# Optimization experiments

Measured on AMD Instinct MI355X. Metric: run time of the kernel, lower is better.

## Reference

```python
import jax, jax.numpy as jnp
import numpy as np

DIM = 1024
EMSIZE = 64  # per-head dim (cfg.emsize = split_size)
N_HEADS = DIM // EMSIZE


def setup_inputs() -> dict:
    key = jax.random.key(0)
    k1, k2, k3 = jax.random.split(key, 3)
    x = jax.random.normal(k1, (4, 2048, DIM), dtype=jnp.float32)
    w_qkv = jax.random.normal(k2, (DIM, 3 * DIM), dtype=jnp.float32) * 0.02
    b_qkv = jnp.zeros((3 * DIM,), dtype=jnp.float32)
    w_proj = jax.random.normal(k3, (DIM, DIM), dtype=jnp.float32) * 0.02
    b_proj = jnp.zeros((DIM,), dtype=jnp.float32)
    return {"x": x, "w_qkv": w_qkv, "b_qkv": b_qkv, "w_proj": w_proj, "b_proj": b_proj}


def reference(x, w_qkv, b_qkv, w_proj, b_proj):
    B, S, D = x.shape
    H, Dh = N_HEADS, EMSIZE
    # QKV projection (Conv1D = affine on last dim)
    qkv = x @ w_qkv + b_qkv                      # [B, S, 3D]
    q, k, v = jnp.split(qkv, 3, axis=-1)
    # split heads: [B, S, H, Dh] -> [B, H, S, Dh]
    q = q.reshape(B, S, H, Dh).transpose(0, 2, 1, 3)
    k = k.reshape(B, S, H, Dh).transpose(0, 2, 1, 3)
    v = v.reshape(B, S, H, Dh).transpose(0, 2, 1, 3)
    # scaled dot-product attention with causal mask (diag included)
    w = jnp.einsum('bhqd,bhkd->bhqk', q, k) / jnp.sqrt(jnp.float32(Dh))
    causal = jnp.arange(S)[None, :] <= jnp.arange(S)[:, None]  # [S, S]
    w = jnp.where(causal[None, None, :, :], w, jnp.float32(-1e9))
    w = jax.nn.softmax(w, axis=-1)
    # dropout is identity at inference
    a = jnp.einsum('bhqk,bhkd->bhqd', w, v)      # [B, H, S, Dh]
    # merge heads
    a = a.transpose(0, 2, 1, 3).reshape(B, S, D)
    # output projection
    return a @ w_proj + b_proj
```

## Files before the change

### kernel.cpp

```cpp
#include <hip/hip_runtime.h>


typedef __bf16 bf16x8 __attribute__((ext_vector_type(8)));
typedef float f32x4 __attribute__((ext_vector_type(4)));
typedef float f32x8 __attribute__((ext_vector_type(8)));
typedef float f32x16 __attribute__((ext_vector_type(16)));
typedef unsigned int u32;
typedef u32 u32x4 __attribute__((ext_vector_type(4)));
typedef unsigned short u16;

#define QSCALE 0.18033688011112042f

__device__ __forceinline__ u16 f2bf(float f) {
  unsigned u = __builtin_bit_cast(unsigned, f);
  return (u16)((u + 0x7FFFu + ((u >> 16) & 1u)) >> 16);
}

__device__ __forceinline__ u32 cvt_pk_bf16(float lo, float hi) {
  u32 r;
  asm("v_cvt_pk_bf16_f32 %0, %1, %2" : "=v"(r) : "v"(lo), "v"(hi));
  return r;
}

__device__ __forceinline__ void gload16(const void* g, void* l) {
  __builtin_amdgcn_global_load_lds(
      (const __attribute__((address_space(1))) unsigned*)g,
      (__attribute__((address_space(3))) unsigned*)l, 16, 0, 0);
}

__global__ __launch_bounds__(256) void k_cvt(const float4* __restrict__ in,
                                             ushort4* __restrict__ out, int n4) {
  int i = blockIdx.x * 256 + threadIdx.x;
  if (i < n4) {
    float4 v = in[i];
    out[i] = make_ushort4(f2bf(v.x), f2bf(v.y), f2bf(v.z), f2bf(v.w));
  }
}

__global__ __launch_bounds__(256) void k_transpose(const float* __restrict__ in,
                                                   u16* __restrict__ out, int R, int C) {
  __shared__ u16 tile[32][33];
  int c0 = blockIdx.x * 32, r0 = blockIdx.y * 32;
  int tx = threadIdx.x & 31, ty = threadIdx.x >> 5;
  for (int i = 0; i < 32; i += 8)
    tile[ty + i][tx] = f2bf(in[(size_t)(r0 + ty + i) * C + c0 + tx]);
  __syncthreads();
  for (int i = 0; i < 32; i += 8)
    out[(size_t)(c0 + ty + i) * R + r0 + tx] = tile[tx][ty + i];
}

template <int MODE>
__global__ __launch_bounds__(256, 2) void k_gemm(
    const u16* __restrict__ A, const u16* __restrict__ Bt,
    const float* __restrict__ bias, float* __restrict__ outF,
    u16* __restrict__ qb, u16* __restrict__ kb, u16* __restrict__ vb,
    int M, int N, int K) {
  __shared__ u16 sA[128 * 32];
  __shared__ u16 sB[128 * 32];
  const int nTn = N >> 7;
  const int tm = blockIdx.x / nTn, tn = blockIdx.x % nTn;
  const int t = threadIdx.x, w = t >> 6, lane = t & 63, g = lane >> 4, c = lane & 15;
  const int wr = w >> 1, wc = w & 1;
  const int rowA0 = tm << 7, colB0 = tn << 7;
  f32x4 acc[4][4] = {};
  const int r = t >> 2, c8 = (t & 3) << 3;
  const u16* gA = A + (size_t)(rowA0 + r) * K + c8;
  const u16* gB = Bt + (size_t)(colB0 + r) * K + c8;
  char* lA = (char*)sA + w * 1024;
  char* lB = (char*)sB + w * 1024;
  for (int k0 = 0; k0 < K; k0 += 32) {
    __syncthreads();
    gload16(gA + k0, lA);
    gload16(gA + k0 + (size_t)64 * K, lA + 4096);
    gload16(gB + k0, lB);
    gload16(gB + k0 + (size_t)64 * K, lB + 4096);
    __syncthreads();
    bf16x8 af[4], bfr[4];
#pragma unroll
    for (int mi = 0; mi < 4; mi++)
      af[mi] = *(const bf16x8*)&sA[(wr * 64 + mi * 16 + c) * 32 + g * 8];
#pragma unroll
    for (int ni = 0; ni < 4; ni++)
      bfr[ni] = *(const bf16x8*)&sB[(wc * 64 + ni * 16 + c) * 32 + g * 8];
#pragma unroll
    for (int mi = 0; mi < 4; mi++)
#pragma unroll
      for (int ni = 0; ni < 4; ni++)
        acc[mi][ni] = __builtin_amdgcn_mfma_f32_16x16x32_bf16(af[mi], bfr[ni], acc[mi][ni], 0, 0, 0);
  }
#pragma unroll
  for (int mi = 0; mi < 4; mi++) {
    int row0 = rowA0 + wr * 64 + mi * 16 + g * 4;
#pragma unroll
    for (int ni = 0; ni < 4; ni++) {
      int col = colB0 + wc * 64 + ni * 16 + c;
      float bv = bias[col];
      if (MODE == 1) {
#pragma unroll
        for (int i = 0; i < 4; i++)
          outF[(size_t)(row0 + i) * N + col] = acc[mi][ni][i] + bv;
      } else {
        int which = col >> 10, cc = col & 1023, h = cc >> 6, d = cc & 63;
        int b_ = row0 >> 11, s = row0 & 2047;
        size_t bh = (size_t)(b_ * 16 + h);
        if (which == 0) {
          u16* dst = qb + (bh * 2048 + s) * 64 + d;
#pragma unroll
          for (int i = 0; i < 4; i++) dst[(size_t)i * 64] = f2bf((acc[mi][ni][i] + bv) * QSCALE);
        } else if (which == 1) {
          u16* dst = kb + (bh * 2048 + s) * 64 + d;
#pragma unroll
          for (int i = 0; i < 4; i++) dst[(size_t)i * 64] = f2bf(acc[mi][ni][i] + bv);
        } else {
          ushort4 pk = make_ushort4(f2bf(acc[mi][ni][0] + bv), f2bf(acc[mi][ni][1] + bv),
                                    f2bf(acc[mi][ni][2] + bv), f2bf(acc[mi][ni][3] + bv));
          *(ushort4*)&vb[(bh * 64 + d) * 2048 + s] = pk;
        }
      }
    }
  }
}

__global__ __launch_bounds__(256, 4) void k_attn(const u16* __restrict__ qb,
                                                 const u16* __restrict__ kb,
                                                 const u16* __restrict__ vb,
                                                 u16* __restrict__ ab) {
  __shared__ u16 sK[2][64 * 64];
  __shared__ u16 sV[2][64 * 64];
  const int bid = blockIdx.x;
  const int qt = 15 - (bid >> 6), bh = bid & 63;
  const int b_ = bh >> 4, hh = bh & 15;
  const int t = threadIdx.x, w = t >> 6, lane = t & 63;
  const int l31 = lane & 31, h = lane >> 5;
  const int q0 = qt << 7, myq = q0 + w * 32;
  const u16* Kg = kb + (size_t)bh * 2048 * 64;
  const u16* Vg = vb + (size_t)bh * 64 * 2048;
  const int rr = t >> 3, p = t & 7;

  const u16* Qrow = qb + ((size_t)bh * 2048 + myq + l31) * 64;
  bf16x8 qf[4];
#pragma unroll
  for (int ks = 0; ks < 4; ks++) qf[ks] = *(const bf16x8*)&Qrow[ks * 16 + h * 8];

#define STAGE(buf, kv0_)                                                      \
  {                                                                           \
    _Pragma("unroll") for (int i = 0; i < 2; i++) {                           \
      int row = i * 32 + rr;                                                  \
      gload16(Kg + ((size_t)(kv0_) + row) * 64 + ((p ^ (row & 7)) << 3),      \
              (char*)sK[buf] + i * 4096 + w * 1024);                          \
      gload16(Vg + (size_t)row * 2048 + (kv0_) + ((p ^ (row & 7)) << 3),      \
              (char*)sV[buf] + i * 4096 + w * 1024);                          \
    }                                                                         \
  }

  f32x16 ot[2] = {};
  float mrun = -__builtin_inff(), lrun = 0.f;
  const int nt = qt * 2 + 2;

  STAGE(0, 0);
  for (int tt = 0; tt < nt; ++tt) {
    const int kv0 = tt << 6;
    __syncthreads();
    if (tt + 1 < nt) STAGE((tt + 1) & 1, kv0 + 64);
    if (kv0 > myq + 31) continue;
    const char* bK = (const char*)sK[tt & 1];
    const char* bV = (const char*)sV[tt & 1];

    f32x16 st[2] = {};
    __builtin_amdgcn_s_setprio(1);
#pragma unroll
    for (int ks = 0; ks < 4; ks++)
#pragma unroll
      for (int kvt = 0; kvt < 2; kvt++) {
        int row = kvt * 32 + l31;
        bf16x8 kf = *(const bf16x8*)(bK + row * 128 + ((ks * 32 + h * 16) ^ ((row & 7) << 4)));
        st[kvt] = __builtin_amdgcn_mfma_f32_32x32x16_bf16(kf, qf[ks], st[kvt], 0, 0, 0);
      }
    __builtin_amdgcn_s_setprio(0);

    if (kv0 + 63 > myq) {
      const int qm = myq + l31 - kv0 - 4 * h;
#pragma unroll
      for (int kvt = 0; kvt < 2; kvt++)
#pragma unroll
        for (int r = 0; r < 16; r++) {
          const int kvo = kvt * 32 + (r & 3) + 8 * (r >> 2);
          st[kvt][r] = (kvo <= qm) ? st[kvt][r] : -__builtin_inff();
        }
    }

    float mt = -__builtin_inff();
#pragma unroll
    for (int r = 0; r < 16; r++) mt = fmaxf(mt, fmaxf(st[0][r], st[1][r]));
    mt = fmaxf(mt, __shfl_xor(mt, 32, 64));
    float mnew = mrun;
    if (!__all(mt <= mrun + 8.f)) {
      mnew = fmaxf(mrun, mt);
      const float corr = __builtin_amdgcn_exp2f(mrun - mnew);
      lrun *= corr;
#pragma unroll
      for (int df = 0; df < 2; df++) ot[df] *= corr;
      mrun = mnew;
    }
#pragma unroll
    for (int kvt = 0; kvt < 2; kvt++)
#pragma unroll
      for (int r = 0; r < 16; r++) st[kvt][r] = __builtin_amdgcn_exp2f(st[kvt][r] - mnew);
    f32x16 ssum = st[0] + st[1];
    f32x8 t8 = __builtin_shufflevector(ssum, ssum, 0, 1, 2, 3, 4, 5, 6, 7) +
               __builtin_shufflevector(ssum, ssum, 8, 9, 10, 11, 12, 13, 14, 15);
    f32x4 t4 = __builtin_shufflevector(t8, t8, 0, 1, 2, 3) +
               __builtin_shufflevector(t8, t8, 4, 5, 6, 7);
    float lt = (t4[0] + t4[1]) + (t4[2] + t4[3]);
    lt += __shfl_xor(lt, 32, 64);
    lrun += lt;

    u32 pk[2][8];
#pragma unroll
    for (int kvt = 0; kvt < 2; kvt++)
#pragma unroll
      for (int j = 0; j < 8; j++)
        pk[kvt][j] = cvt_pk_bf16(st[kvt][2 * j], st[kvt][2 * j + 1]);
    __builtin_amdgcn_s_setprio(1);
#pragma unroll
    for (int s = 0; s < 4; s++) {
      const int kvf = s >> 1, jb = (s & 1) * 4;
      const u32 XloW0 = pk[kvf][jb + 0], XloW1 = pk[kvf][jb + 1];
      const u32 XhiW0 = pk[kvf][jb + 2], XhiW1 = pk[kvf][jb + 3];
      const u32 cHi0 = (u32)__shfl_xor((int)XhiW0, 32, 64);
      const u32 cHi1 = (u32)__shfl_xor((int)XhiW1, 32, 64);
      const u32 cLo0 = (u32)__shfl_xor((int)XloW0, 32, 64);
      const u32 cLo1 = (u32)__shfl_xor((int)XloW1, 32, 64);
      u32x4 pw;
      pw[0] = h ? cHi0 : XloW0;
      pw[1] = h ? cHi1 : XloW1;
      pw[2] = h ? XhiW0 : cLo0;
      pw[3] = h ? XhiW1 : cLo1;
      const bf16x8 pf = __builtin_bit_cast(bf16x8, pw);
#pragma unroll
      for (int df = 0; df < 2; df++) {
        const int row = df * 32 + l31;
        bf16x8 vf = *(const bf16x8*)(bV + row * 128 + ((s * 32 + h * 16) ^ ((row & 7) << 4)));
        ot[df] = __builtin_amdgcn_mfma_f32_32x32x16_bf16(vf, pf, ot[df], 0, 0, 0);
      }
    }
    __builtin_amdgcn_s_setprio(0);
  }

  const float inv = 1.f / lrun;
  u16* Arow = ab + ((size_t)b_ * 2048 + myq + l31) * 1024 + hh * 64;
#pragma unroll
  for (int df = 0; df < 2; df++)
#pragma unroll
    for (int qd = 0; qd < 4; qd++) {
      const int d0 = df * 32 + qd * 8 + h * 4;
      ushort4 pkv = make_ushort4(f2bf(ot[df][qd * 4 + 0] * inv), f2bf(ot[df][qd * 4 + 1] * inv),
                                 f2bf(ot[df][qd * 4 + 2] * inv), f2bf(ot[df][qd * 4 + 3] * inv));
      *(ushort4*)&Arow[d0] = pkv;
    }
#undef STAGE
}

extern "C" void kernel_launch(void* const* d_in, const int* in_sizes, int n_in,
                              void* d_out, int out_size, void* d_ws, size_t ws_size,
                              hipStream_t stream) {
  const float* x = (const float*)d_in[0];
  const float* w_qkv = (const float*)d_in[1];
  const float* b_qkv = (const float*)d_in[2];
  const float* w_proj = (const float*)d_in[3];
  const float* b_proj = (const float*)d_in[4];

  u16* xb = (u16*)d_ws;
  u16* wqkvT = xb + (size_t)8192 * 1024;
  u16* wprojT = wqkvT + (size_t)3072 * 1024;
  u16* qb = wprojT + (size_t)1024 * 1024;
  u16* kb = qb + (size_t)8192 * 1024;
  u16* vb = kb + (size_t)8192 * 1024;
  u16* ab = xb;

  k_cvt<<<8192, 256, 0, stream>>>((const float4*)x, (ushort4*)xb, 8192 * 1024 / 4);
  k_transpose<<<dim3(3072 / 32, 1024 / 32), 256, 0, stream>>>(w_qkv, wqkvT, 1024, 3072);
  k_transpose<<<dim3(1024 / 32, 1024 / 32), 256, 0, stream>>>(w_proj, wprojT, 1024, 1024);
  k_gemm<0><<<(8192 / 128) * (3072 / 128), 256, 0, stream>>>(
      xb, wqkvT, b_qkv, nullptr, qb, kb, vb, 8192, 3072, 1024);
  k_attn<<<1024, 256, 0, stream>>>(qb, kb, vb, ab);
  k_gemm<1><<<(8192 / 128) * (1024 / 128), 256, 0, stream>>>(
      ab, wprojT, b_proj, (float*)d_out, nullptr, nullptr, nullptr, 8192, 1024, 1024);
}
```

Baseline: 260.8 us.

## Replace QKV GEMM with 256x256-tile double-buffered ping-pong MFMA kernel

```diff
diff --git a/kernel.cpp b/kernel.cpp
--- a/kernel.cpp
+++ b/kernel.cpp
@@ -49,11 +49,150 @@
     out[(size_t)(c0 + ty + i) * R + r0 + tx] = tile[tx][ty + i];
 }
 
+__global__ __launch_bounds__(512, 2) void k_gemm256(
+    const u16* __restrict__ A, const u16* __restrict__ Bt,
+    const float* __restrict__ bias,
+    u16* __restrict__ qb, u16* __restrict__ kb, u16* __restrict__ vb, int K) {
+  __shared__ u16 lds[2][2][2][8192];
+  const int b0 = blockIdx.x;
+  const int bsw = (b0 & 7) * 48 + (b0 >> 3);
+  const int tm = bsw / 12, tn = bsw % 12;
+  const int t = threadIdx.x, w = t >> 6, lane = t & 63;
+  const int wm = w >> 2, wn = w & 3, hb = wn >> 1;
+  const int cls = wm * 2 + hb;
+  const int l31 = lane & 31, h8 = lane >> 5;
+  const int sg8 = ((lane & 7) ^ (lane >> 3)) << 3;
+  const int NT = K >> 6;
+  const u16* Ag = A + (size_t)tm * 256 * K;
+  const u16* Bg = Bt + (size_t)tn * 256 * K;
+
+  f32x16 acc[4][2] = {};
+  bf16x8 aR[4][4], bR[2][4];
+
+#define STAGE_HALF(P, Tn)                                                     \
+  {                                                                           \
+    const u16* gb = ((P)&1) ? Bg : Ag;                                        \
+    _Pragma("unroll") for (int r = 0; r < 2; r++) {                           \
+      int row = r * 64 + w * 8 + (lane >> 3);                                 \
+      gload16(gb + (size_t)(((P) >> 1) * 128 + row) * K + (Tn)*64 + sg8,      \
+              (char*)&lds[(Tn)&1][(P)&1][(P) >> 1][0] + r * 8192 + w * 1024); \
+    }                                                                         \
+  }
+#define LDA(mg)                                                                \
+  _Pragma("unroll") for (int mf = (mg)*2; mf < (mg)*2 + 2; mf++)               \
+  _Pragma("unroll") for (int ks = 0; ks < 4; ks++)                             \
+    aR[mf][ks] = *(const bf16x8*)(Abase + (mf * 32 + l31) * 128 +              \
+                                  (((ks * 2 + h8) ^ (l31 & 7)) << 4));
+#define LDB(nf)                                                                \
+  _Pragma("unroll") for (int ks = 0; ks < 4; ks++)                             \
+    bR[nf][ks] = *(const bf16x8*)(Bbase + ((wn & 1) * 64 + (nf)*32 + l31) * 128 + \
+                                  (((ks * 2 + h8) ^ (l31 & 7)) << 4));
+#define MQ(mg, nf)                                                             \
+  {                                                                            \
+    __builtin_amdgcn_s_setprio(1);                                             \
+    _Pragma("unroll") for (int mf = (mg)*2; mf < (mg)*2 + 2; mf++)             \
+    _Pragma("unroll") for (int ks = 0; ks < 4; ks++)                           \
+      acc[mf][nf] = __builtin_amdgcn_mfma_f32_32x32x16_bf16(                   \
+          aR[mf][ks], bR[nf][ks], acc[mf][nf], 0, 0, 0);                       \
+    __builtin_amdgcn_s_setprio(0);                                             \
+  }
+#define PH(P, QBODY)                                                           \
+  {                                                                            \
+    if (T + 1 < NT) {                                                          \
+      STAGE_HALF(P, T + 1);                                                    \
+      asm volatile("s_waitcnt vmcnt(6)" ::: "memory");                         \
+    } else {                                                                   \
+      if ((P) == 0) asm volatile("s_waitcnt vmcnt(4)" ::: "memory");           \
+      else if ((P) == 1) asm volatile("s_waitcnt vmcnt(2)" ::: "memory");      \
+      else if ((P) == 2) asm volatile("s_waitcnt vmcnt(0)" ::: "memory");      \
+    }                                                                          \
+    __builtin_amdgcn_sched_barrier(0);                                         \
+    __builtin_amdgcn_s_barrier();                                              \
+    __builtin_amdgcn_sched_barrier(0);                                         \
+    const char* Abase = (const char*)&lds[T & 1][0][wm][0];                    \
+    const char* Bbase = (const char*)&lds[T & 1][1][hb][0];                    \
+    (void)Abase; (void)Bbase;                                                  \
+    QBODY                                                                      \
+    asm volatile("s_waitcnt lgkmcnt(0)" ::: "memory");                         \
+    __builtin_amdgcn_sched_barrier(0);                                         \
+    __builtin_amdgcn_s_barrier();                                              \
+    __builtin_amdgcn_sched_barrier(0);                                         \
+  }
+
+  STAGE_HALF(0, 0);
+  STAGE_HALF(1, 0);
+  STAGE_HALF(2, 0);
+  STAGE_HALF(3, 0);
+
+  for (int T = 0; T < NT; ++T) {
+    PH(0, {
+      if (cls == 0)      { LDA(0); LDB(0); MQ(0, 0); }
+      else if (cls == 2) { if (T) MQ(1, 0); }
+      else               { if (T) MQ(1, 1); }
+    })
+    PH(1, {
+      if (cls == 0)      { LDB(1); MQ(0, 1); }
+      else if (cls == 2) { LDA(0); LDB(0); MQ(0, 0); }
+      else               { if (T) MQ(1, 0); }
+    })
+    PH(2, {
+      if (cls == 0)      { LDA(1); MQ(1, 1); }
+      else if (cls == 2) { LDB(1); MQ(0, 1); }
+      else               { LDA(0); LDB(0); MQ(0, 0); }
+    })
+    PH(3, {
+      if (cls == 0)      { MQ(1, 0); }
+      else if (cls == 2) { LDA(1); MQ(1, 1); }
+      else               { LDA(1); LDB(1); MQ(0, 1); }
+    })
+  }
+  if (cls == 2) { MQ(1, 0); }
+  else if (cls == 1 || cls == 3) { MQ(1, 1); MQ(1, 0); }
+
+  const int which = tn >> 2;
+#pragma unroll
+  for (int mf = 0; mf < 4; mf++) {
+    const int rb = tm * 256 + wm * 128 + mf * 32 + 4 * h8;
+    const int b_ = rb >> 11, sB = rb & 2047;
+#pragma unroll
+    for (int nf = 0; nf < 2; nf++) {
+      const int cl = tn * 256 + wn * 64 + nf * 32 + l31;
+      const float bv = bias[cl];
+      const int hd = (cl >> 6) & 15, d = cl & 63;
+      const size_t bh = (size_t)(b_ * 16 + hd);
+      if (which == 0) {
+        u16* dst = qb + (bh * 2048 + sB) * 64 + d;
+#pragma unroll
+        for (int r = 0; r < 16; r++)
+          dst[(size_t)((r & 3) + 8 * (r >> 2)) * 64] = f2bf((acc[mf][nf][r] + bv) * QSCALE);
+      } else if (which == 1) {
+        u16* dst = kb + (bh * 2048 + sB) * 64 + d;
+#pragma unroll
+        for (int r = 0; r < 16; r++)
+          dst[(size_t)((r & 3) + 8 * (r >> 2)) * 64] = f2bf(acc[mf][nf][r] + bv);
+      } else {
+        u16* dst = vb + (bh * 64 + d) * 2048 + sB;
+#pragma unroll
+        for (int rq = 0; rq < 4; rq++) {
+          ushort4 pk = make_ushort4(
+              f2bf(acc[mf][nf][rq * 4 + 0] + bv), f2bf(acc[mf][nf][rq * 4 + 1] + bv),
+              f2bf(acc[mf][nf][rq * 4 + 2] + bv), f2bf(acc[mf][nf][rq * 4 + 3] + bv));
+          *(ushort4*)&dst[rq * 8] = pk;
+        }
+      }
+    }
+  }
+#undef STAGE_HALF
+#undef LDA
+#undef LDB
+#undef MQ
+#undef PH
+}
+
 template <int MODE>
 __global__ __launch_bounds__(256, 2) void k_gemm(
     const u16* __restrict__ A, const u16* __restrict__ Bt,
     const float* __restrict__ bias, float* __restrict__ outF,
-    u16* __restrict__ qb, u16* __restrict__ kb, u16* __restrict__ vb,
     int M, int N, int K) {
   __shared__ u16 sA[128 * 32];
   __shared__ u16 sB[128 * 32];
@@ -95,28 +234,9 @@
     for (int ni = 0; ni < 4; ni++) {
       int col = colB0 + wc * 64 + ni * 16 + c;
       float bv = bias[col];
-      if (MODE == 1) {
-#pragma unroll
-        for (int i = 0; i < 4; i++)
-          outF[(size_t)(row0 + i) * N + col] = acc[mi][ni][i] + bv;
-      } else {
-        int which = col >> 10, cc = col & 1023, h = cc >> 6, d = cc & 63;
-        int b_ = row0 >> 11, s = row0 & 2047;
-        size_t bh = (size_t)(b_ * 16 + h);
-        if (which == 0) {
-          u16* dst = qb + (bh * 2048 + s) * 64 + d;
-#pragma unroll
-          for (int i = 0; i < 4; i++) dst[(size_t)i * 64] = f2bf((acc[mi][ni][i] + bv) * QSCALE);
-        } else if (which == 1) {
-          u16* dst = kb + (bh * 2048 + s) * 64 + d;
-#pragma unroll
-          for (int i = 0; i < 4; i++) dst[(size_t)i * 64] = f2bf(acc[mi][ni][i] + bv);
-        } else {
-          ushort4 pk = make_ushort4(f2bf(acc[mi][ni][0] + bv), f2bf(acc[mi][ni][1] + bv),
-                                    f2bf(acc[mi][ni][2] + bv), f2bf(acc[mi][ni][3] + bv));
-          *(ushort4*)&vb[(bh * 64 + d) * 2048 + s] = pk;
-        }
-      }
+#pragma unroll
+      for (int i = 0; i < 4; i++)
+        outF[(size_t)(row0 + i) * N + col] = acc[mi][ni][i] + bv;
     }
   }
 }
@@ -281,9 +401,8 @@
   k_cvt<<<8192, 256, 0, stream>>>((const float4*)x, (ushort4*)xb, 8192 * 1024 / 4);
   k_transpose<<<dim3(3072 / 32, 1024 / 32), 256, 0, stream>>>(w_qkv, wqkvT, 1024, 3072);
   k_transpose<<<dim3(1024 / 32, 1024 / 32), 256, 0, stream>>>(w_proj, wprojT, 1024, 1024);
-  k_gemm<0><<<(8192 / 128) * (3072 / 128), 256, 0, stream>>>(
-      xb, wqkvT, b_qkv, nullptr, qb, kb, vb, 8192, 3072, 1024);
+  k_gemm256<<<384, 512, 0, stream>>>(xb, wqkvT, b_qkv, qb, kb, vb, 1024);
   k_attn<<<1024, 256, 0, stream>>>(qb, kb, vb, ab);
   k_gemm<1><<<(8192 / 128) * (1024 / 128), 256, 0, stream>>>(
-      ab, wprojT, b_proj, (float*)d_out, nullptr, nullptr, nullptr, 8192, 1024, 1024);
-}
+      ab, wprojT, b_proj, (float*)d_out, 8192, 1024, 1024);
+}
```

Measured after the change: 267.2 us. 1.02x slower.

## Replace QKV GEMM with 256x256-tile double-buffered 32x32 MFMA kernel

Applied to the files above, without the earlier changes.

```diff
diff --git a/kernel.cpp b/kernel.cpp
--- a/kernel.cpp
+++ b/kernel.cpp
@@ -49,11 +49,130 @@
     out[(size_t)(c0 + ty + i) * R + r0 + tx] = tile[tx][ty + i];
 }
 
+__global__ __launch_bounds__(512, 2) void k_gemm256(
+    const u16* __restrict__ A, const u16* __restrict__ Bt,
+    const float* __restrict__ bias,
+    u16* __restrict__ qb, u16* __restrict__ kb, u16* __restrict__ vb) {
+  const int K = 1024, NT = 16;
+  __shared__ u16 lds[2][2][2][8192];
+  const int b0 = blockIdx.x;
+  const int bsw = (b0 & 7) * 48 + (b0 >> 3);
+  const int tm = bsw / 12, tn = bsw % 12;
+  const int t = threadIdx.x, w = t >> 6, lane = t & 63;
+  const int wm = w >> 2, wn = w & 3, hb = wn >> 1;
+  const int l31 = lane & 31, h8 = lane >> 5;
+  const int sg8 = ((lane & 7) ^ ((lane >> 3) & 7)) << 3;
+  const u16* Ag = A + (size_t)tm * 256 * K;
+  const u16* Bg = Bt + (size_t)tn * 256 * K;
+
+  f32x16 acc[4][2] = {};
+  bf16x8 aR[4][4], bR[2][4];
+
+#define STG(ab, hf, Tn, BUF)                                                \
+  { const u16* gb = (ab) ? Bg : Ag;                                         \
+    _Pragma("unroll") for (int r = 0; r < 2; r++) {                         \
+      int row = r * 64 + w * 8 + ((lane >> 3) & 7);                         \
+      gload16(gb + (size_t)((hf)*128 + row) * K + (size_t)(Tn)*64 + sg8,    \
+              (char*)&lds[BUF][ab][hf][0] + r * 8192 + w * 1024);           \
+    } }
+#define RDA(mf, BUF)                                                        \
+  _Pragma("unroll") for (int ks = 0; ks < 4; ks++)                          \
+    aR[mf][ks] = *(const bf16x8*)((const char*)&lds[BUF][0][wm][0] +        \
+        ((mf)*32 + l31) * 128 + (((ks * 2 + h8) ^ (l31 & 7)) << 4));
+#define RDB(nf, BUF)                                                        \
+  _Pragma("unroll") for (int ks = 0; ks < 4; ks++)                          \
+    bR[nf][ks] = *(const bf16x8*)((const char*)&lds[BUF][1][hb][0] +        \
+        (((wn & 1) * 64 + (nf)*32 + l31)) * 128 +                           \
+        (((ks * 2 + h8) ^ (l31 & 7)) << 4));
+#define MQ(mg, nf)                                                          \
+  { __builtin_amdgcn_s_setprio(1);                                         \
+    _Pragma("unroll") for (int ks = 0; ks < 4; ks++) {                      \
+      acc[(mg)*2][nf] = __builtin_amdgcn_mfma_f32_32x32x16_bf16(            \
+          aR[(mg)*2][ks], bR[nf][ks], acc[(mg)*2][nf], 0, 0, 0);            \
+      acc[(mg)*2 + 1][nf] = __builtin_amdgcn_mfma_f32_32x32x16_bf16(        \
+          aR[(mg)*2 + 1][ks], bR[nf][ks], acc[(mg)*2 + 1][nf], 0, 0, 0);    \
+    }                                                                       \
+    __builtin_amdgcn_s_setprio(0); }
+#define BAR()                                                               \
+  { __builtin_amdgcn_sched_barrier(0); __builtin_amdgcn_s_barrier();        \
+    __builtin_amdgcn_sched_barrier(0); }
+
+  STG(0, 0, 0, 0) STG(0, 1, 0, 0) STG(1, 0, 0, 0) STG(1, 1, 0, 0)
+  STG(0, 0, 1, 1) STG(0, 1, 1, 1) STG(1, 0, 1, 1) STG(1, 1, 1, 1)
+  asm volatile("s_waitcnt vmcnt(8)" ::: "memory");
+  BAR();
+
+#define TILE(T, BUF)                                                        \
+  {                                                                 \
+    RDA(0, BUF) RDA(1, BUF) RDB(0, BUF)                                     \
+    BAR(); MQ(0, 0) BAR();                                                  \
+                                                                    \
+    RDA(2, BUF) RDA(3, BUF)                                                 \
+    BAR(); MQ(1, 0) BAR();                                                  \
+                                                                    \
+    RDB(1, BUF)                                                             \
+    if ((T) + 2 < NT) { STG(0, 0, (T) + 2, BUF) STG(0, 1, (T) + 2, BUF) }   \
+    BAR(); MQ(0, 1) BAR();                                                  \
+                                                                    \
+    if ((T) + 2 < NT) { STG(1, 0, (T) + 2, BUF) STG(1, 1, (T) + 2, BUF) }   \
+    BAR(); MQ(1, 1)                                                         \
+    if ((T) < NT - 2) {                                                     \
+      asm volatile("s_waitcnt vmcnt(8)" ::: "memory");                      \
+    } else if ((T) == NT - 2) {                                             \
+      asm volatile("s_waitcnt vmcnt(0)" ::: "memory");                      \
+    }                                                                       \
+    BAR(); }
+
+  for (int Tp = 0; Tp < NT; Tp += 2) {
+    TILE(Tp, 0)
+    TILE(Tp + 1, 1)
+  }
+
+  const int which = tn >> 2;
+#pragma unroll
+  for (int mf = 0; mf < 4; mf++) {
+    const int rb = tm * 256 + wm * 128 + mf * 32 + 4 * h8;
+    const int b_ = rb >> 11, sB = rb & 2047;
+#pragma unroll
+    for (int nf = 0; nf < 2; nf++) {
+      const int cl = tn * 256 + wn * 64 + nf * 32 + l31;
+      const float bv = bias[cl];
+      const int hd = (cl >> 6) & 15, d = cl & 63;
+      const size_t bh = (size_t)(b_ * 16 + hd);
+      if (which == 0) {
+        u16* dst = qb + (bh * 2048 + sB) * 64 + d;
+#pragma unroll
+        for (int r = 0; r < 16; r++)
+          dst[(size_t)((r & 3) + 8 * (r >> 2)) * 64] = f2bf((acc[mf][nf][r] + bv) * QSCALE);
+      } else if (which == 1) {
+        u16* dst = kb + (bh * 2048 + sB) * 64 + d;
+#pragma unroll
+        for (int r = 0; r < 16; r++)
+          dst[(size_t)((r & 3) + 8 * (r >> 2)) * 64] = f2bf(acc[mf][nf][r] + bv);
+      } else {
+        u16* dst = vb + (bh * 64 + d) * 2048 + sB;
+#pragma unroll
+        for (int rq = 0; rq < 4; rq++) {
+          ushort4 pk = make_ushort4(
+              f2bf(acc[mf][nf][rq * 4 + 0] + bv), f2bf(acc[mf][nf][rq * 4 + 1] + bv),
+              f2bf(acc[mf][nf][rq * 4 + 2] + bv), f2bf(acc[mf][nf][rq * 4 + 3] + bv));
+          *(ushort4*)&dst[rq * 8] = pk;
+        }
+      }
+    }
+  }
+#undef STG
+#undef RDA
+#undef RDB
+#undef MQ
+#undef BAR
+#undef TILE
+}
+
 template <int MODE>
 __global__ __launch_bounds__(256, 2) void k_gemm(
     const u16* __restrict__ A, const u16* __restrict__ Bt,
     const float* __restrict__ bias, float* __restrict__ outF,
-    u16* __restrict__ qb, u16* __restrict__ kb, u16* __restrict__ vb,
     int M, int N, int K) {
   __shared__ u16 sA[128 * 32];
   __shared__ u16 sB[128 * 32];
@@ -95,28 +214,9 @@
     for (int ni = 0; ni < 4; ni++) {
       int col = colB0 + wc * 64 + ni * 16 + c;
       float bv = bias[col];
-      if (MODE == 1) {
-#pragma unroll
-        for (int i = 0; i < 4; i++)
-          outF[(size_t)(row0 + i) * N + col] = acc[mi][ni][i] + bv;
-      } else {
-        int which = col >> 10, cc = col & 1023, h = cc >> 6, d = cc & 63;
-        int b_ = row0 >> 11, s = row0 & 2047;
-        size_t bh = (size_t)(b_ * 16 + h);
-        if (which == 0) {
-          u16* dst = qb + (bh * 2048 + s) * 64 + d;
-#pragma unroll
-          for (int i = 0; i < 4; i++) dst[(size_t)i * 64] = f2bf((acc[mi][ni][i] + bv) * QSCALE);
-        } else if (which == 1) {
-          u16* dst = kb + (bh * 2048 + s) * 64 + d;
-#pragma unroll
-          for (int i = 0; i < 4; i++) dst[(size_t)i * 64] = f2bf(acc[mi][ni][i] + bv);
-        } else {
-          ushort4 pk = make_ushort4(f2bf(acc[mi][ni][0] + bv), f2bf(acc[mi][ni][1] + bv),
-                                    f2bf(acc[mi][ni][2] + bv), f2bf(acc[mi][ni][3] + bv));
-          *(ushort4*)&vb[(bh * 64 + d) * 2048 + s] = pk;
-        }
-      }
+#pragma unroll
+      for (int i = 0; i < 4; i++)
+        outF[(size_t)(row0 + i) * N + col] = acc[mi][ni][i] + bv;
     }
   }
 }
@@ -281,9 +381,8 @@
   k_cvt<<<8192, 256, 0, stream>>>((const float4*)x, (ushort4*)xb, 8192 * 1024 / 4);
   k_transpose<<<dim3(3072 / 32, 1024 / 32), 256, 0, stream>>>(w_qkv, wqkvT, 1024, 3072);
   k_transpose<<<dim3(1024 / 32, 1024 / 32), 256, 0, stream>>>(w_proj, wprojT, 1024, 1024);
-  k_gemm<0><<<(8192 / 128) * (3072 / 128), 256, 0, stream>>>(
-      xb, wqkvT, b_qkv, nullptr, qb, kb, vb, 8192, 3072, 1024);
+  k_gemm256<<<384, 512, 0, stream>>>(xb, wqkvT, b_qkv, qb, kb, vb);
   k_attn<<<1024, 256, 0, stream>>>(qb, kb, vb, ab);
   k_gemm<1><<<(8192 / 128) * (1024 / 128), 256, 0, stream>>>(
-      ab, wprojT, b_proj, (float*)d_out, nullptr, nullptr, nullptr, 8192, 1024, 1024);
-}
+      ab, wprojT, b_proj, (float*)d_out, 8192, 1024, 1024);
+}
```

After: 266.8 us. 2.3% more time.
